# Kernel tuning notes

Hardware: AMD Instinct MI355X
Metric: run time of the kernel (lower is better)

## Reference

```python
import jax, jax.numpy as jnp
import numpy as np

D_MODEL = 3072
N_HEADS = 24
MAX_LEN = 2048
ROPE_THETA = 10000.0
DH = D_MODEL // N_HEADS                  # 128
Q_PROJ = D_MODEL // 2                    # 1536
KV_PROJ = 2 * D_MODEL // 3               # 2048
NOPE = DH // 2                           # 64
ROPE = DH // 2                           # 64
EPS = 1e-5


def layernorm(x, w, b):
    m = jnp.mean(x, axis=-1, keepdims=True)
    v = jnp.mean(jnp.square(x - m), axis=-1, keepdims=True)
    return (x - m) / jnp.sqrt(v + EPS) * w + b


def rotate_half(x):
    h = x.shape[-1] // 2
    return jnp.concatenate([-x[..., h:], x[..., :h]], axis=-1)


def rope_tables(S):
    freqs = 1.0 / ROPE_THETA ** (jnp.arange(0, DH, 2, dtype=jnp.float32) / DH)  # [DH/2]
    emb = jnp.arange(S, dtype=jnp.float32)[:, None] * freqs[None, :]            # [S, DH/2]
    # torch: take first ROPE//2 freqs then .repeat(...,2) => tile along last axis
    cos = jnp.tile(jnp.cos(emb)[:, : ROPE // 2], (1, 2))  # [S, ROPE]
    sin = jnp.tile(jnp.sin(emb)[:, : ROPE // 2], (1, 2))
    return cos[None, None], sin[None, None]               # [1,1,S,ROPE]


def setup_inputs() -> dict:
    key = jax.random.key(0)
    ks = jax.random.split(key, 7)
    x = jax.random.normal(ks[0], (2, 2048, D_MODEL), dtype=jnp.float32)
    p = lambda k, shp: 0.01 * jax.random.normal(k, shp, dtype=jnp.float32)
    return {
        "x": x,
        "W_dq": p(ks[1], (D_MODEL, Q_PROJ)),
        "W_uq": p(ks[2], (Q_PROJ, D_MODEL)),
        "q_ln_w": jnp.ones((Q_PROJ,), jnp.float32),
        "q_ln_b": jnp.zeros((Q_PROJ,), jnp.float32),
        "W_dkv": p(ks[3], (D_MODEL, KV_PROJ + ROPE)),
        "W_ukv": p(ks[4], (KV_PROJ, D_MODEL + N_HEADS * NOPE)),
        "kv_ln_w": jnp.ones((KV_PROJ,), jnp.float32),
        "kv_ln_b": jnp.zeros((KV_PROJ,), jnp.float32),
        "W_o": p(ks[5], (D_MODEL, D_MODEL)),
    }


def reference(x, W_dq, W_uq, q_ln_w, q_ln_b, W_dkv, W_ukv, kv_ln_w, kv_ln_b, W_o):
    B, S, D = x.shape
    cos, sin = rope_tables(S)  # past_length=0, S_full=S

    # Q path: low-rank down/up projection
    cq = layernorm(x @ W_dq, q_ln_w, q_ln_b)          # [B,S,Q_PROJ]
    Q = (cq @ W_uq).reshape(B, S, N_HEADS, DH).transpose(0, 2, 1, 3)  # [B,H,S,DH]
    Q_nope, Q_rope = Q[..., :NOPE], Q[..., NOPE:]
    Q_rope = Q_rope * cos + rotate_half(Q_rope) * sin

    # KV path
    compressed_kv = x @ W_dkv                          # [B,S,KV_PROJ+ROPE]
    KV_lora = layernorm(compressed_kv[..., :KV_PROJ], kv_ln_w, kv_ln_b)
    K_rope = compressed_kv[..., KV_PROJ:]              # [B,S,ROPE]
    KV = (KV_lora @ W_ukv).reshape(B, S, N_HEADS, DH + NOPE).transpose(0, 2, 1, 3)
    K_nope, V = KV[..., :NOPE], KV[..., NOPE:]         # [B,H,S,NOPE], [B,H,S,DH]

    K_rope = K_rope[:, None]                           # [B,1,S,ROPE] shared head
    K_rope = K_rope * cos + rotate_half(K_rope) * sin

    q = jnp.concatenate([Q_nope, Q_rope], axis=-1)     # [B,H,S,DH]
    # k = cat(K_nope, K_rope broadcast over heads)
    k = jnp.concatenate([K_nope, jnp.broadcast_to(K_rope, (B, N_HEADS, S, ROPE))], axis=-1)

    scale = 1.0 / jnp.sqrt(jnp.float32(DH))
    scores = jnp.einsum("bhqd,bhkd->bhqk", q, k) * scale
    causal = jnp.tril(jnp.ones((S, S), dtype=bool))
    scores = jnp.where(causal[None, None], scores, jnp.float32(-jnp.inf))
    attn = jax.nn.softmax(scores, axis=-1)
    out = jnp.einsum("bhqk,bhkd->bhqd", attn, V)
    out = out.transpose(0, 2, 1, 3).reshape(B, S, D)
    out = out @ W_o.T
    return out, compressed_kv
```

## Files before the change

### kernel.cpp

```cpp
#include <hip/hip_runtime.h>

typedef unsigned short u16;
typedef __attribute__((ext_vector_type(8))) short short8;
typedef __attribute__((ext_vector_type(4))) float f32x4;

#define NROWS   4096
#define S_LEN   2048
#define NHEADS  24
#define DMODEL  3072
#define QPROJ   1536
#define KVPROJ  2048
#define CKV_W   2112
#define UKV_N   4608

__device__ __forceinline__ float bf2f(u16 v) {
    unsigned u = ((unsigned)v) << 16; float f; __builtin_memcpy(&f, &u, 4); return f;
}
__device__ __forceinline__ u16 f2bf(float f) {
    unsigned u; __builtin_memcpy(&u, &f, 4);
    u = (u + 0x7FFFu + ((u >> 16) & 1u)) >> 16; return (u16)u;
}
__device__ __forceinline__ void async16(const u16* g, u16* l) {
    __builtin_amdgcn_global_load_lds((const __attribute__((address_space(1))) unsigned int*)g,
                                     (__attribute__((address_space(3))) unsigned int*)l,
                                     16, 0, 0);
}

__global__ void conv_bf16(const float* __restrict__ X, u16* __restrict__ Y, int n) {
    int i = (blockIdx.x * 256 + threadIdx.x) * 4;
    if (i >= n) return;
    float4 v = *(const float4*)(X + i);
    Y[i+0] = f2bf(v.x); Y[i+1] = f2bf(v.y); Y[i+2] = f2bf(v.z); Y[i+3] = f2bf(v.w);
}

__global__ void transpose_bf16(const float* __restrict__ W, u16* __restrict__ WT,
                               int K, int N, float scale) {
    __shared__ float t[32][33];
    int nb = blockIdx.x * 32, kb = blockIdx.y * 32;
    int c = threadIdx.x & 31, rq = threadIdx.x >> 5;
#pragma unroll
    for (int i = 0; i < 4; ++i) {
        int r = rq * 4 + i;
        t[r][c] = W[(size_t)(kb + r) * N + nb + c];
    }
    __syncthreads();
#pragma unroll
    for (int i = 0; i < 4; ++i) {
        int r = rq * 4 + i;
        WT[(size_t)(nb + r) * K + kb + c] = f2bf(t[c][r] * scale);
    }
}

__global__ __launch_bounds__(256) void ln_kernel(const float* __restrict__ X, int ldx,
                                                 const float* __restrict__ g,
                                                 const float* __restrict__ b,
                                                 u16* __restrict__ Y, int W) {
    int row = blockIdx.x;
    const float* x = X + (size_t)row * ldx;
    float s = 0.f, s2 = 0.f;
    for (int i = threadIdx.x; i < W; i += 256) { float v = x[i]; s += v; s2 += v * v; }
#pragma unroll
    for (int off = 32; off >= 1; off >>= 1) { s += __shfl_xor(s, off); s2 += __shfl_xor(s2, off); }
    __shared__ float red[8];
    int w = threadIdx.x >> 6;
    if ((threadIdx.x & 63) == 0) { red[w] = s; red[4 + w] = s2; }
    __syncthreads();
    s  = red[0] + red[1] + red[2] + red[3];
    s2 = red[4] + red[5] + red[6] + red[7];
    float mean = s / W;
    float var  = s2 / W - mean * mean;
    float rstd = rsqrtf(var + 1e-5f);
    u16* y = Y + (size_t)row * W;
    for (int i = threadIdx.x; i < W; i += 256)
        y[i] = f2bf((x[i] - mean) * rstd * g[i] + b[i]);
}

__global__ void rope_q_kernel(u16* __restrict__ Q) {
    int idx = blockIdx.x * 256 + threadIdx.x;
    int j = idx & 31; int t = idx >> 5; int h = t % NHEADS; int row = t / NHEADS;
    int s = row & (S_LEN - 1);
    float freq = __expf(-(float)j * (9.210340371976184f / 64.f));
    float ang = (float)s * freq;
    float c = cosf(ang), si = sinf(ang);
    u16* p = Q + (size_t)row * DMODEL + h * 128 + 64;
    float x1 = bf2f(p[j]), x2 = bf2f(p[j + 32]);
    p[j]      = f2bf(x1 * c - x2 * si);
    p[j + 32] = f2bf(x2 * c + x1 * si);
}

__global__ void rope_k_kernel(const float* __restrict__ ckv, u16* __restrict__ kr) {
    int idx = blockIdx.x * 256 + threadIdx.x;
    int j = idx & 31; int row = idx >> 5;
    int s = row & (S_LEN - 1);
    float freq = __expf(-(float)j * (9.210340371976184f / 64.f));
    float ang = (float)s * freq;
    float c = cosf(ang), si = sinf(ang);
    const float* src = ckv + (size_t)row * CKV_W + KVPROJ;
    float x1 = src[j], x2 = src[j + 32];
    kr[(size_t)row * 64 + j]      = f2bf(x1 * c - x2 * si);
    kr[(size_t)row * 64 + j + 32] = f2bf(x2 * c + x1 * si);
}

__global__ __launch_bounds__(256) void pack_k(const u16* __restrict__ KVb,
                                              const u16* __restrict__ kr,
                                              u16* __restrict__ Kp) {
    int bh = blockIdx.y, bb = bh / NHEADS, h = bh % NHEADS;
    int s0 = blockIdx.x * 64;
    int t = threadIdx.x;
    size_t base = (size_t)bb * S_LEN;
#pragma unroll
    for (int it = 0; it < 4; ++it) {
        int j = it * 256 + t;
        int r = j >> 4, cb = (j & 15) * 8;
        int s = s0 + r;
        uint4 v;
        if (cb < 64) v = *(const uint4*)&KVb[(base + s) * UKV_N + h * 192 + cb];
        else         v = *(const uint4*)&kr[(base + s) * 64 + (cb - 64)];
        *(uint4*)&Kp[((size_t)bh * S_LEN + s) * 128 + cb] = v;
    }
}

__global__ __launch_bounds__(256) void pack_v(const u16* __restrict__ KVb,
                                              u16* __restrict__ Vt) {
    __shared__ u16 tile[64][136];
    int bh = blockIdx.y, bb = bh / NHEADS, h = bh % NHEADS;
    int s0 = blockIdx.x * 64;
    int t = threadIdx.x;
    size_t base = (size_t)bb * S_LEN;
#pragma unroll
    for (int it = 0; it < 4; ++it) {
        int j = it * 256 + t;
        int r = j >> 4, cb = (j & 15) * 8;
        *(uint4*)&tile[r][cb] = *(const uint4*)&KVb[(base + s0 + r) * UKV_N + h * 192 + 64 + cb];
    }
    __syncthreads();
#pragma unroll
    for (int it = 0; it < 4; ++it) {
        int j = it * 256 + t;
        int d = j >> 3, sb = (j & 7) * 8;
        u16 tmp[8];
#pragma unroll
        for (int e = 0; e < 8; ++e) tmp[e] = tile[sb + e][d];
        *(uint4*)&Vt[((size_t)bh * 128 + d) * S_LEN + s0 + sb] = *(uint4*)tmp;
    }
}

template<bool OUT_BF16>
__global__ __launch_bounds__(256) void gemm_nt(const u16* __restrict__ A,
                                               const u16* __restrict__ B,
                                               void* __restrict__ Cv,
                                               int M, int N, int K) {
    __shared__ u16 a_lds[2][128][32];
    __shared__ u16 b_lds[2][128][32];
    int m0 = blockIdx.y * 128, n0 = blockIdx.x * 128;
    int tid = threadIdx.x, lane = tid & 63, w = tid >> 6;
    int wm = w >> 1, wn = w & 1;
    int srow = lane >> 2;
    int kx = (lane >> 4) & 2;
    int scol = ((lane & 3) ^ kx) * 8;
    int r0 = w * 32 + srow, r1 = w * 32 + 16 + srow;
    const u16* A0 = A + (size_t)(m0 + r0) * K + scol;
    const u16* A1 = A + (size_t)(m0 + r1) * K + scol;
    int bn0 = n0 + r0; if (bn0 >= N) bn0 = N - 1;
    int bn1 = n0 + r1; if (bn1 >= N) bn1 = N - 1;
    const u16* B0 = B + (size_t)bn0 * K + scol;
    const u16* B1 = B + (size_t)bn1 * K + scol;
    char* aB = (char*)&a_lds[0][0][0];
    char* bB = (char*)&b_lds[0][0][0];
    int d0 = w * 2048, d1 = w * 2048 + 1024;
    int cb = ((lane >> 4) * 16) ^ ((lane & 8) << 2);

    f32x4 acc[4][4] = {};
    async16(A0, (u16*)(aB + d0)); async16(A1, (u16*)(aB + d1));
    async16(B0, (u16*)(bB + d0)); async16(B1, (u16*)(bB + d1));
    __syncthreads();
    int buf = 0;
    for (int kb = 0; kb < K; kb += 32) {
        if (kb + 32 < K) {
            int ob = (buf ^ 1) * 8192;
            async16(A0 + kb + 32, (u16*)(aB + ob + d0));
            async16(A1 + kb + 32, (u16*)(aB + ob + d1));
            async16(B0 + kb + 32, (u16*)(bB + ob + d0));
            async16(B1 + kb + 32, (u16*)(bB + ob + d1));
        }
        const char* ab = aB + buf * 8192;
        const char* bb = bB + buf * 8192;
        short8 af[4], bf[4];
#pragma unroll
        for (int i = 0; i < 4; ++i) {
            af[i] = *(const short8*)(ab + (wm * 64 + i * 16 + (lane & 15)) * 64 + cb);
            bf[i] = *(const short8*)(bb + (wn * 64 + i * 16 + (lane & 15)) * 64 + cb);
        }
#pragma unroll
        for (int i = 0; i < 4; ++i)
#pragma unroll
            for (int j = 0; j < 4; ++j)
                acc[i][j] = __builtin_amdgcn_mfma_f32_16x16x32_bf16(af[i], bf[j], acc[i][j], 0, 0, 0);
        __syncthreads();
        buf ^= 1;
    }
#pragma unroll
    for (int i = 0; i < 4; ++i) {
        int row = m0 + wm * 64 + i * 16 + ((lane >> 4) << 2);
#pragma unroll
        for (int j = 0; j < 4; ++j) {
            int col = n0 + wn * 64 + j * 16 + (lane & 15);
            if (col < N) {
#pragma unroll
                for (int r = 0; r < 4; ++r) {
                    if (OUT_BF16) ((u16*)Cv)[(size_t)(row + r) * N + col] = f2bf(acc[i][j][r]);
                    else          ((float*)Cv)[(size_t)(row + r) * N + col] = acc[i][j][r];
                }
            }
        }
    }
}

__global__ __launch_bounds__(512) void attn_kernel(const u16* __restrict__ Qb,
                                                   const u16* __restrict__ Kp,
                                                   const u16* __restrict__ Vt,
                                                   u16* __restrict__ AO) {
    __shared__ u16 k_lds[64][128];
    __shared__ u16 v_lds[128][64];
    __shared__ u16 p_lds[8][16][72];
    int qxb = (int)gridDim.x - 1 - (int)blockIdx.x;
    int q0 = qxb * 128;
    int bh = blockIdx.y; int bb = bh / NHEADS, h = bh % NHEADS;
    int tid = threadIdx.x, lane = tid & 63, w = tid >> 6;
    size_t base = (size_t)bb * S_LEN;
    size_t bhS = (size_t)bh * S_LEN;

    short8 qf[4];
    {
        int qrow = q0 + w * 16 + (lane & 15);
        const u16* qp = Qb + (base + qrow) * DMODEL + h * 128 + ((lane >> 4) * 8);
#pragma unroll
        for (int ks = 0; ks < 4; ++ks) qf[ks] = *(const short8*)(qp + ks * 32);
    }

    const char* Kbyte = (const char*)Kp;
    const char* Vbyte = (const char*)Vt;
    char* kB = (char*)&k_lds[0][0];
    char* vB = (char*)&v_lds[0][0];
    size_t ksrc[2], vsrc[2];
    int kd[2];
#pragma unroll
    for (int is = 0; is < 2; ++is) {
        int j = is * 512 + tid;
        int r = j >> 4;
        int cbs = ((j & 15) * 16) ^ ((r & 7) << 4);
        ksrc[is] = (bhS + r) * 256 + cbs;
        int d = j >> 3;
        int kbs = (((j & 7) ^ (d & 7)) * 16);
        vsrc[is] = ((size_t)bh * 128 + d) * (S_LEN * 2) + kbs;
        kd[is] = (is * 512 + w * 64) * 16;
    }

    f32x4 acc_o[8] = {};
    float m_run[4], l_run[4];
#pragma unroll
    for (int r = 0; r < 4; ++r) { m_run[r] = -1e30f; l_run[r] = 0.f; }

    int ntiles = 2 * qxb + 2;
    int wave_nt = ((q0 + w * 16 + 15) >> 6) + 1;

    for (int t = 0; t < ntiles; ++t) {
        size_t kv0 = (size_t)t * 64;
#pragma unroll
        for (int is = 0; is < 2; ++is)
            async16((const u16*)(Kbyte + ksrc[is] + kv0 * 256), (u16*)(kB + kd[is]));
#pragma unroll
        for (int is = 0; is < 2; ++is)
            async16((const u16*)(Vbyte + vsrc[is] + kv0 * 2), (u16*)(vB + kd[is]));
        __syncthreads();

        if (t < wave_nt) {
            f32x4 sc[4];
            __builtin_amdgcn_s_setprio(1);
#pragma unroll
            for (int nb = 0; nb < 4; ++nb) {
                f32x4 a = {};
                int row = nb * 16 + (lane & 15);
                const char* kb_ = kB + row * 256;
                int x = (row & 7) << 4;
#pragma unroll
                for (int ks = 0; ks < 4; ++ks) {
                    short8 kf = *(const short8*)(kb_ + ((ks * 64 + (lane >> 4) * 16) ^ x));
                    a = __builtin_amdgcn_mfma_f32_16x16x32_bf16(qf[ks], kf, a, 0, 0, 0);
                }
                sc[nb] = a;
            }
            __builtin_amdgcn_s_setprio(0);

            if (t + 1 == wave_nt) {
                int kvb = t * 64;
                int qg = q0 + w * 16 + ((lane >> 4) << 2);
#pragma unroll
                for (int nb = 0; nb < 4; ++nb) {
                    int kc = kvb + nb * 16 + (lane & 15);
#pragma unroll
                    for (int r = 0; r < 4; ++r)
                        if (kc > qg + r) sc[nb][r] = -1e30f;
                }
            }
            float rmax[4];
#pragma unroll
            for (int r = 0; r < 4; ++r)
                rmax[r] = fmaxf(fmaxf(sc[0][r], sc[1][r]), fmaxf(sc[2][r], sc[3][r]));
#pragma unroll
            for (int off = 1; off < 16; off <<= 1)
#pragma unroll
                for (int r = 0; r < 4; ++r) rmax[r] = fmaxf(rmax[r], __shfl_xor(rmax[r], off));

            float mnew[4], fac[4], rsum[4];
#pragma unroll
            for (int r = 0; r < 4; ++r) {
                mnew[r] = fmaxf(m_run[r], rmax[r]);
                fac[r] = __expf(m_run[r] - mnew[r]);
                rsum[r] = 0.f;
            }
#pragma unroll
            for (int nb = 0; nb < 4; ++nb)
#pragma unroll
                for (int r = 0; r < 4; ++r) {
                    float p = __expf(sc[nb][r] - mnew[r]);
                    sc[nb][r] = p; rsum[r] += p;
                }
#pragma unroll
            for (int off = 1; off < 16; off <<= 1)
#pragma unroll
                for (int r = 0; r < 4; ++r) rsum[r] += __shfl_xor(rsum[r], off);
#pragma unroll
            for (int r = 0; r < 4; ++r) {
                l_run[r] = l_run[r] * fac[r] + rsum[r];
                m_run[r] = mnew[r];
            }
#pragma unroll
            for (int db = 0; db < 8; ++db)
#pragma unroll
                for (int r = 0; r < 4; ++r) acc_o[db][r] *= fac[r];

#pragma unroll
            for (int nb = 0; nb < 4; ++nb)
#pragma unroll
                for (int r = 0; r < 4; ++r)
                    p_lds[w][((lane >> 4) << 2) + r][nb * 16 + (lane & 15)] = f2bf(sc[nb][r]);
            __builtin_amdgcn_sched_barrier(0);
            __builtin_amdgcn_s_setprio(1);
#pragma unroll
            for (int ks = 0; ks < 2; ++ks) {
                short8 pf = *(const short8*)&p_lds[w][lane & 15][ks * 32 + (lane >> 4) * 8];
#pragma unroll
                for (int db = 0; db < 8; ++db) {
                    int row = db * 16 + (lane & 15);
                    const char* vb_ = vB + row * 128;
                    short8 vf = *(const short8*)(vb_ + ((ks * 64 + (lane >> 4) * 16) ^ ((row & 7) << 4)));
                    acc_o[db] = __builtin_amdgcn_mfma_f32_16x16x32_bf16(pf, vf, acc_o[db], 0, 0, 0);
                }
            }
            __builtin_amdgcn_s_setprio(0);
        }
        __syncthreads();
    }

    int orow = q0 + w * 16 + ((lane >> 4) << 2);
#pragma unroll
    for (int db = 0; db < 8; ++db)
#pragma unroll
        for (int r = 0; r < 4; ++r) {
            float o = acc_o[db][r] / l_run[r];
            AO[(base + orow + r) * DMODEL + h * 128 + db * 16 + (lane & 15)] = f2bf(o);
        }
}

extern "C" void kernel_launch(void* const* d_in, const int* in_sizes, int n_in,
                              void* d_out, int out_size, void* d_ws, size_t ws_size,
                              hipStream_t stream) {
    (void)in_sizes; (void)n_in; (void)out_size; (void)ws_size;
    const float* x      = (const float*)d_in[0];
    const float* W_dq   = (const float*)d_in[1];
    const float* W_uq   = (const float*)d_in[2];
    const float* q_ln_w = (const float*)d_in[3];
    const float* q_ln_b = (const float*)d_in[4];
    const float* W_dkv  = (const float*)d_in[5];
    const float* W_ukv  = (const float*)d_in[6];
    const float* kv_ln_w= (const float*)d_in[7];
    const float* kv_ln_b= (const float*)d_in[8];
    const float* W_o    = (const float*)d_in[9];

    float* out = (float*)d_out;
    float* ckv = out + (size_t)NROWS * DMODEL;

    char* ws = (char*)d_ws;
    const size_t OFF_WDQT  = 0;
    const size_t OFF_WUQT  = 9437184;
    const size_t OFF_WDKVT = 18874368;
    const size_t OFF_WUKVT = 31850496;
    const size_t OFF_WO    = 50724864;
    const size_t OFF_XB    = 69599232;
    const size_t OFF_QB    = 94765056;
    const size_t OFF_KVB   = 119930880;
    const size_t OFF_KR    = 157679616;
    const size_t OFF_SLABA = 158203904;
    const size_t OFF_SLABB = 183369728;
    const size_t OFF_KP    = 0;
    const size_t OFF_VT    = OFF_XB;

    u16* Wdq_t  = (u16*)(ws + OFF_WDQT);
    u16* Wuq_t  = (u16*)(ws + OFF_WUQT);
    u16* Wdkv_t = (u16*)(ws + OFF_WDKVT);
    u16* Wukv_t = (u16*)(ws + OFF_WUKVT);
    u16* Wo_b   = (u16*)(ws + OFF_WO);
    u16* xb     = (u16*)(ws + OFF_XB);
    u16* qb     = (u16*)(ws + OFF_QB);
    u16* KVb    = (u16*)(ws + OFF_KVB);
    u16* kr     = (u16*)(ws + OFF_KR);
    float* t0   = (float*)(ws + OFF_SLABA);
    u16* ao     = (u16*)(ws + OFF_SLABA);
    u16* cq     = (u16*)(ws + OFF_SLABB);
    u16* kvl    = (u16*)(ws + OFF_SLABB);
    u16* Kp     = (u16*)(ws + OFF_KP);
    u16* Vt     = (u16*)(ws + OFF_VT);

    const float SCALE = 0.08838834764831845f;

    transpose_bf16<<<dim3(QPROJ / 32, DMODEL / 32), 256, 0, stream>>>(W_dq,  Wdq_t,  DMODEL, QPROJ, 1.0f);
    transpose_bf16<<<dim3(DMODEL / 32, QPROJ / 32), 256, 0, stream>>>(W_uq,  Wuq_t,  QPROJ, DMODEL, SCALE);
    transpose_bf16<<<dim3(CKV_W / 32, DMODEL / 32), 256, 0, stream>>>(W_dkv, Wdkv_t, DMODEL, CKV_W, 1.0f);
    transpose_bf16<<<dim3(UKV_N / 32, KVPROJ / 32), 256, 0, stream>>>(W_ukv, Wukv_t, KVPROJ, UKV_N, 1.0f);
    conv_bf16<<<9216, 256, 0, stream>>>(W_o, Wo_b, DMODEL * DMODEL);
    conv_bf16<<<12288, 256, 0, stream>>>(x, xb, NROWS * DMODEL);

    gemm_nt<false><<<dim3(QPROJ / 128, NROWS / 128), 256, 0, stream>>>(xb, Wdq_t, t0, NROWS, QPROJ, DMODEL);
    ln_kernel<<<NROWS, 256, 0, stream>>>(t0, QPROJ, q_ln_w, q_ln_b, cq, QPROJ);
    gemm_nt<true><<<dim3(DMODEL / 128, NROWS / 128), 256, 0, stream>>>(cq, Wuq_t, qb, NROWS, DMODEL, QPROJ);
    rope_q_kernel<<<12288, 256, 0, stream>>>(qb);

    gemm_nt<false><<<dim3((CKV_W + 127) / 128, NROWS / 128), 256, 0, stream>>>(xb, Wdkv_t, ckv, NROWS, CKV_W, DMODEL);
    ln_kernel<<<NROWS, 256, 0, stream>>>(ckv, CKV_W, kv_ln_w, kv_ln_b, kvl, KVPROJ);
    rope_k_kernel<<<512, 256, 0, stream>>>(ckv, kr);
    gemm_nt<true><<<dim3(UKV_N / 128, NROWS / 128), 256, 0, stream>>>(kvl, Wukv_t, KVb, NROWS, UKV_N, KVPROJ);

    pack_k<<<dim3(S_LEN / 64, 2 * NHEADS), 256, 0, stream>>>(KVb, kr, Kp);
    pack_v<<<dim3(S_LEN / 64, 2 * NHEADS), 256, 0, stream>>>(KVb, Vt);

    attn_kernel<<<dim3(S_LEN / 128, 2 * NHEADS), 512, 0, stream>>>(qb, Kp, Vt, ao);

    gemm_nt<false><<<dim3(DMODEL / 128, NROWS / 128), 256, 0, stream>>>(ao, Wo_b, out, NROWS, DMODEL, DMODEL);
}
```

Before: 702.3 us.

## Restructure causal attention into paired 64-row q blocks with lazy rescaling

```diff
diff --git a/kernel.cpp b/kernel.cpp
--- a/kernel.cpp
+++ b/kernel.cpp
@@ -216,65 +216,68 @@
     }
 }
 
-__global__ __launch_bounds__(512) void attn_kernel(const u16* __restrict__ Qb,
+__global__ __launch_bounds__(256) void attn_kernel(const u16* __restrict__ Qb,
                                                    const u16* __restrict__ Kp,
                                                    const u16* __restrict__ Vt,
                                                    u16* __restrict__ AO) {
     __shared__ u16 k_lds[64][128];
     __shared__ u16 v_lds[128][64];
-    __shared__ u16 p_lds[8][16][72];
-    int qxb = (int)gridDim.x - 1 - (int)blockIdx.x;
-    int q0 = qxb * 128;
-    int bh = blockIdx.y; int bb = bh / NHEADS, h = bh % NHEADS;
+    __shared__ u16 p_lds[4][16][72];
+    int bid = blockIdx.x;
+    int jj = bid >> 3;
+    int bh = (bid & 7) * 6 + (jj >> 4);
+    int bx = jj & 15;
+    int bb = bh / NHEADS, h = bh % NHEADS;
     int tid = threadIdx.x, lane = tid & 63, w = tid >> 6;
     size_t base = (size_t)bb * S_LEN;
     size_t bhS = (size_t)bh * S_LEN;
-
-    short8 qf[4];
-    {
-        int qrow = q0 + w * 16 + (lane & 15);
-        const u16* qp = Qb + (base + qrow) * DMODEL + h * 128 + ((lane >> 4) * 8);
-#pragma unroll
-        for (int ks = 0; ks < 4; ++ks) qf[ks] = *(const short8*)(qp + ks * 32);
-    }
 
     const char* Kbyte = (const char*)Kp;
     const char* Vbyte = (const char*)Vt;
     char* kB = (char*)&k_lds[0][0];
     char* vB = (char*)&v_lds[0][0];
-    size_t ksrc[2], vsrc[2];
-    int kd[2];
-#pragma unroll
-    for (int is = 0; is < 2; ++is) {
-        int j = is * 512 + tid;
+    size_t ksrc[4], vsrc[4];
+    int kd[4];
+#pragma unroll
+    for (int is = 0; is < 4; ++is) {
+        int j = is * 256 + tid;
         int r = j >> 4;
         int cbs = ((j & 15) * 16) ^ ((r & 7) << 4);
         ksrc[is] = (bhS + r) * 256 + cbs;
         int d = j >> 3;
         int kbs = (((j & 7) ^ (d & 7)) * 16);
         vsrc[is] = ((size_t)bh * 128 + d) * (S_LEN * 2) + kbs;
-        kd[is] = (is * 512 + w * 64) * 16;
-    }
-
-    f32x4 acc_o[8] = {};
-    float m_run[4], l_run[4];
-#pragma unroll
-    for (int r = 0; r < 4; ++r) { m_run[r] = -1e30f; l_run[r] = 0.f; }
-
-    int ntiles = 2 * qxb + 2;
-    int wave_nt = ((q0 + w * 16 + 15) >> 6) + 1;
-
-    for (int t = 0; t < ntiles; ++t) {
-        size_t kv0 = (size_t)t * 64;
-#pragma unroll
-        for (int is = 0; is < 2; ++is)
-            async16((const u16*)(Kbyte + ksrc[is] + kv0 * 256), (u16*)(kB + kd[is]));
-#pragma unroll
-        for (int is = 0; is < 2; ++is)
-            async16((const u16*)(Vbyte + vsrc[is] + kv0 * 2), (u16*)(vB + kd[is]));
-        __syncthreads();
-
-        if (t < wave_nt) {
+        kd[is] = (is * 256 + w * 64) * 16;
+    }
+
+    for (int seg = 0; seg < 2; ++seg) {
+        int qx = seg == 0 ? (31 - bx) : bx;
+        int q0 = qx * 64;
+
+        short8 qf[4];
+        {
+            int qrow = q0 + w * 16 + (lane & 15);
+            const u16* qp = Qb + (base + qrow) * DMODEL + h * 128 + ((lane >> 4) * 8);
+#pragma unroll
+            for (int ks = 0; ks < 4; ++ks) qf[ks] = *(const short8*)(qp + ks * 32);
+        }
+
+        f32x4 acc_o[8] = {};
+        float m_run[4], l_run[4];
+#pragma unroll
+        for (int r = 0; r < 4; ++r) { m_run[r] = -1e30f; l_run[r] = 0.f; }
+
+        int ntiles = qx + 1;
+        for (int t = 0; t < ntiles; ++t) {
+            size_t kv0 = (size_t)t * 64;
+#pragma unroll
+            for (int is = 0; is < 4; ++is)
+                async16((const u16*)(Kbyte + ksrc[is] + kv0 * 256), (u16*)(kB + kd[is]));
+#pragma unroll
+            for (int is = 0; is < 4; ++is)
+                async16((const u16*)(Vbyte + vsrc[is] + kv0 * 2), (u16*)(vB + kd[is]));
+            __syncthreads();
+
             f32x4 sc[4];
             __builtin_amdgcn_s_setprio(1);
 #pragma unroll
@@ -292,7 +295,7 @@
             }
             __builtin_amdgcn_s_setprio(0);
 
-            if (t + 1 == wave_nt) {
+            if (t == qx) {
                 int kvb = t * 64;
                 int qg = q0 + w * 16 + ((lane >> 4) << 2);
 #pragma unroll
@@ -312,18 +315,28 @@
 #pragma unroll
                 for (int r = 0; r < 4; ++r) rmax[r] = fmaxf(rmax[r], __shfl_xor(rmax[r], off));
 
-            float mnew[4], fac[4], rsum[4];
-#pragma unroll
-            for (int r = 0; r < 4; ++r) {
-                mnew[r] = fmaxf(m_run[r], rmax[r]);
-                fac[r] = __expf(m_run[r] - mnew[r]);
-                rsum[r] = 0.f;
-            }
+            bool ok = (rmax[0] <= m_run[0]) & (rmax[1] <= m_run[1]) &
+                      (rmax[2] <= m_run[2]) & (rmax[3] <= m_run[3]);
+            if (!__all(ok)) {
+                float fac[4];
+#pragma unroll
+                for (int r = 0; r < 4; ++r) {
+                    float mnew = fmaxf(m_run[r], rmax[r]);
+                    fac[r] = __expf(m_run[r] - mnew);
+                    m_run[r] = mnew;
+                    l_run[r] *= fac[r];
+                }
+#pragma unroll
+                for (int db = 0; db < 8; ++db)
+#pragma unroll
+                    for (int r = 0; r < 4; ++r) acc_o[db][r] *= fac[r];
+            }
+            float rsum[4] = {0.f, 0.f, 0.f, 0.f};
 #pragma unroll
             for (int nb = 0; nb < 4; ++nb)
 #pragma unroll
                 for (int r = 0; r < 4; ++r) {
-                    float p = __expf(sc[nb][r] - mnew[r]);
+                    float p = __expf(sc[nb][r] - m_run[r]);
                     sc[nb][r] = p; rsum[r] += p;
                 }
 #pragma unroll
@@ -331,14 +344,7 @@
 #pragma unroll
                 for (int r = 0; r < 4; ++r) rsum[r] += __shfl_xor(rsum[r], off);
 #pragma unroll
-            for (int r = 0; r < 4; ++r) {
-                l_run[r] = l_run[r] * fac[r] + rsum[r];
-                m_run[r] = mnew[r];
-            }
-#pragma unroll
-            for (int db = 0; db < 8; ++db)
-#pragma unroll
-                for (int r = 0; r < 4; ++r) acc_o[db][r] *= fac[r];
+            for (int r = 0; r < 4; ++r) l_run[r] += rsum[r];
 
 #pragma unroll
             for (int nb = 0; nb < 4; ++nb)
@@ -359,18 +365,18 @@
                 }
             }
             __builtin_amdgcn_s_setprio(0);
+            __syncthreads();
         }
-        __syncthreads();
-    }
-
-    int orow = q0 + w * 16 + ((lane >> 4) << 2);
-#pragma unroll
-    for (int db = 0; db < 8; ++db)
-#pragma unroll
-        for (int r = 0; r < 4; ++r) {
-            float o = acc_o[db][r] / l_run[r];
-            AO[(base + orow + r) * DMODEL + h * 128 + db * 16 + (lane & 15)] = f2bf(o);
-        }
+
+        int orow = q0 + w * 16 + ((lane >> 4) << 2);
+#pragma unroll
+        for (int db = 0; db < 8; ++db)
+#pragma unroll
+            for (int r = 0; r < 4; ++r) {
+                float o = acc_o[db][r] / l_run[r];
+                AO[(base + orow + r) * DMODEL + h * 128 + db * 16 + (lane & 15)] = f2bf(o);
+            }
+    }
 }
 
 extern "C" void kernel_launch(void* const* d_in, const int* in_sizes, int n_in,
@@ -444,7 +450,7 @@
     pack_k<<<dim3(S_LEN / 64, 2 * NHEADS), 256, 0, stream>>>(KVb, kr, Kp);
     pack_v<<<dim3(S_LEN / 64, 2 * NHEADS), 256, 0, stream>>>(KVb, Vt);
 
-    attn_kernel<<<dim3(S_LEN / 128, 2 * NHEADS), 512, 0, stream>>>(qb, Kp, Vt, ao);
+    attn_kernel<<<768, 256, 0, stream>>>(qb, Kp, Vt, ao);
 
     gemm_nt<false><<<dim3(DMODEL / 128, NROWS / 128), 256, 0, stream>>>(ao, Wo_b, out, NROWS, DMODEL, DMODEL);
 }
```

Result: faster. 672.4 us (-4.3%).
